# Kernel tuning notes

Hardware: AMD Instinct MI355X
Metric: run time of the kernel (lower is better)

## Reference

```python
import jax, jax.numpy as jnp
import numpy as np

N = 128
HID = 512
NUM_IRREPS = 7

_ISO = np.array([
    [1,0,1,0,0,0,0],
    [0,1,0,1,1,0,0],
    [1,0,1,0,0,0,0],
    [0,1,0,1,1,0,0],
    [0,1,0,1,1,0,0],
    [0,0,0,0,0,1,0],
    [0,0,0,0,0,0,1],
], dtype=np.float32)


def setup_inputs() -> dict:
    key = jax.random.key(0)
    k1, k2 = jax.random.split(key)
    x = jax.random.normal(k1, (2, N, N, HID), dtype=jnp.float32)
    # xavier_uniform with relu gain on [num_irreps, num_irreps]
    gain = float(np.sqrt(2.0))
    bound = gain * float(np.sqrt(6.0 / (NUM_IRREPS + NUM_IRREPS)))
    weight = jax.random.uniform(k2, (NUM_IRREPS, NUM_IRREPS), dtype=jnp.float32,
                                minval=-bound, maxval=bound)
    iso_matrix = jnp.asarray(_ISO)
    return {"x": x, "weight": weight, "iso_matrix": iso_matrix}


def _decompose(M):
    # M: [h, n, n] -> [7, h, n, n], isotypic components under S_n conjugation.
    n = M.shape[-1]
    eye = jnp.eye(n, dtype=M.dtype)
    off = 1.0 - eye
    d = jnp.diagonal(M, axis1=-2, axis2=-1)                 # [h, n]
    dbar = jnp.mean(d, axis=-1, keepdims=True)              # [h, 1]
    P1 = dbar[..., None] * eye                              # diag mean (trivial)
    P2 = (d - dbar)[..., None] * eye                        # diag deviation (standard)
    O = M * off                                             # off-diagonal part
    s = jnp.sum(O, axis=(-2, -1)) / (n * (n - 1))           # [h]
    P3 = s[..., None, None] * off                           # offdiag mean (trivial)
    Op = O - P3
    r = jnp.sum(Op, axis=-1)                                # row sums, [h, n]
    c = jnp.sum(Op, axis=-2)                                # col sums, [h, n]
    xr = ((n - 1) * r + c) / (n * (n - 2))
    yc = ((n - 1) * c + r) / (n * (n - 2))
    P4 = xr[..., :, None] * off                             # row standard copy
    P5 = yc[..., None, :] * off                             # col standard copy
    R = Op - P4 - P5                                        # zero diag / row / col sums
    Rt = jnp.swapaxes(R, -1, -2)
    P6 = 0.5 * (R + Rt)                                     # irrep (n-2,2)
    P7 = 0.5 * (R - Rt)                                     # irrep (n-2,1,1)
    return jnp.stack([P1, P2, P3, P4, P5, P6, P7])          # [7, h, n, n]


def reference(x, weight, iso_matrix):
    # x: [2, n, n, hidden] -> transpose(1,3): [2, hidden, n, n]
    xt = jnp.transpose(x, (0, 3, 2, 1))
    A, B = xt[0], xt[1]                                     # [h, n, n]
    params = weight * iso_matrix                            # [7, 7]
    a = _decompose(A)                                       # [7, h, n, n]
    b = _decompose(B)
    # params @ comps, then sum over output irrep axis (fused into one einsum)
    A_out = jnp.einsum('ij,jhmn->hmn', params, a)
    B_out = jnp.einsum('ij,jhmn->hmn', params, b)
    out = jnp.stack([A_out, B_out])                         # [2, h, n, n]
    return jnp.transpose(out, (0, 3, 2, 1))                 # [2, n, n, hidden]
```

## Files before the change

kernel.cpp:

```cpp
#include <hip/hip_runtime.h>
#include <math.h>

#define N 128
#define HID 512
#define NH (N * HID)
#define SNH ((size_t)N * NH)
#define NPAIRS (N * (N + 1) / 2)

#define OFF_PSC 0
#define OFF_PSR 4194304
#define OFF_DG  4718592
#define OFF_XR  4849664
#define OFF_YC  4980736
#define OFF_SV  5111808
#define OFF_DB  5112832

typedef float vf4 __attribute__((ext_vector_type(4)));
union F4 { vf4 v; float f[4]; };

__global__ __launch_bounds__(512)
void schur_p1(const float* __restrict__ x, float* __restrict__ PScol,
              float* __restrict__ PSrow, float* __restrict__ Dg) {
    const int u  = blockIdx.x;
    const int hq = u & 3;
    const int bq = (u >> 2) & 3;
    const int g  = (u >> 4) & 7;
    const int s  = u >> 7;
    const int tid = threadIdx.x;
    const int f   = tid & 31;
    const int bg  = tid >> 5;
    const int b0  = bq * 32 + bg * 2;
    const int hoff = hq * 128 + f * 4;

    const float* xs   = x + (size_t)s * SNH;
    const float* base = xs + (size_t)(g * 16) * NH + b0 * HID + hoff;

    __shared__ F4 rowred[8][16][32];

    F4 acc0, acc1;
    acc0.v = (vf4)(0.f); acc1.v = (vf4)(0.f);

    #pragma unroll
    for (int c = 0; c < 2; ++c) {
        #pragma unroll
        for (int al = 0; al < 8; ++al) {
            const float* p = base + (size_t)(c * 8 + al) * NH;
            F4 v0; v0.v = *reinterpret_cast<const vf4*>(p);
            F4 v1; v1.v = *reinterpret_cast<const vf4*>(p + HID);
            acc0.v += v0.v;
            acc1.v += v1.v;
            F4 rs; rs.v = v0.v + v1.v;
            rowred[al][bg][f] = rs;
        }
        __syncthreads();
        if (tid < 256) {
            const int ar = tid >> 5;
            const int f2 = tid & 31;
            F4 t; t.v = (vf4)(0.f);
            #pragma unroll
            for (int k = 0; k < 16; ++k) t.v += rowred[ar][k][f2].v;
            const int a = g * 16 + c * 8 + ar;
            *reinterpret_cast<vf4*>(PSrow +
                ((((size_t)s * 4 + bq) * N + a) * HID + hq * 128 + f2 * 4)) = t.v;
        }
        __syncthreads();
    }

    *reinterpret_cast<vf4*>(PScol +
        ((((size_t)s * 8 + g) * N + b0) * HID + hoff)) = acc0.v;
    *reinterpret_cast<vf4*>(PScol +
        ((((size_t)s * 8 + g) * N + b0 + 1) * HID + hoff)) = acc1.v;

    if (bq == (g >> 1)) {
        const int ar = tid >> 5;
        const int f2 = tid & 31;
        const int a  = g * 16 + ar;
        const vf4 dv = *reinterpret_cast<const vf4*>(
            xs + (size_t)a * NH + a * HID + hq * 128 + f2 * 4);
        *reinterpret_cast<vf4*>(Dg +
            (((size_t)s * N + a) * HID + hq * 128 + f2 * 4)) = dv;
    }
}

__global__ __launch_bounds__(512)
void schur_p2(const float* __restrict__ PScol, const float* __restrict__ PSrow,
              const float* __restrict__ Dg,
              float* __restrict__ Xr, float* __restrict__ Yc,
              float* __restrict__ Sv, float* __restrict__ Db) {
    const int bi = blockIdx.x;
    const int s  = bi >> 4;
    const int hc = bi & 15;
    const int t  = threadIdx.x;
    const int iq = t >> 5;
    const int hl = t & 31;
    const int h  = hc * 32 + hl;

    float sa8[8], sb8[8], d8[8];
    float T = 0.f, D = 0.f;
    #pragma unroll
    for (int k = 0; k < 8; ++k) {
        const int i = iq + k * 16;
        float sa = 0.f, sb = 0.f;
        #pragma unroll
        for (int gg = 0; gg < 8; ++gg)
            sa += PScol[(((size_t)s * 8 + gg) * N + i) * HID + h];
        #pragma unroll
        for (int qq = 0; qq < 4; ++qq)
            sb += PSrow[(((size_t)s * 4 + qq) * N + i) * HID + h];
        const float d = Dg[((size_t)s * N + i) * HID + h];
        sa8[k] = sa; sb8[k] = sb; d8[k] = d;
        T += sa; D += d;
    }

    __shared__ float redT[16][32];
    __shared__ float redD[16][32];
    __shared__ float shS[32];
    redT[iq][hl] = T;
    redD[iq][hl] = D;
    __syncthreads();
    if (iq == 0) {
        float Tt = 0.f, Dd = 0.f;
        #pragma unroll
        for (int q = 0; q < 16; ++q) { Tt += redT[q][hl]; Dd += redD[q][hl]; }
        const float sh   = (Tt - Dd) * (1.0f / 16256.0f);
        const float dbar = Dd * (1.0f / 128.0f);
        Sv[s * HID + h] = sh;
        Db[s * HID + h] = dbar;
        shS[hl] = sh;
    }
    __syncthreads();

    const float sh    = shS[hl];
    const float k127s = 127.0f * sh;
    const float inv   = 1.0f / 16128.0f;
    const size_t base = (size_t)s * N * HID;
    #pragma unroll
    for (int k = 0; k < 8; ++k) {
        const int i = iq + k * 16;
        const float d = d8[k];
        const float r = sa8[k] - d - k127s;
        const float c = sb8[k] - d - k127s;
        Xr[base + (size_t)i * HID + h] = (127.0f * r + c) * inv;
        Yc[base + (size_t)i * HID + h] = (127.0f * c + r) * inv;
    }
}

__global__ __launch_bounds__(256)
void schur_p3(const float* __restrict__ x, const float* __restrict__ w,
              const float* __restrict__ iso,
              const float* __restrict__ Xr, const float* __restrict__ Yc,
              const float* __restrict__ Sv, const float* __restrict__ Db,
              float* __restrict__ out) {
    const int t  = threadIdx.x;
    const int k  = t >> 7;
    const int ht = t & 127;
    const int hoff = ht * 4;

    float c[7];
    #pragma unroll
    for (int j = 0; j < 7; ++j) {
        float acc = 0.f;
        #pragma unroll
        for (int i = 0; i < 7; ++i) acc += w[i * 7 + j] * iso[i * 7 + j];
        c[j] = acc;
    }
    const float c1 = c[0], c2 = c[1], c3 = c[2], c4 = c[3], c5 = c[4];
    const float al = 0.5f * (c[5] + c[6]);
    const float be = 0.5f * (c[5] - c[6]);

    const int pg0 = blockIdx.x * 8;

    #define TRI_OFF(aa) ((aa) * N - (((aa) * ((aa) - 1)) >> 1))
    #pragma unroll
    for (int it = 0; it < 4; ++it) {
        const int pg = pg0 + it * 2 + k;
        const int s  = (pg >= NPAIRS) ? 1 : 0;
        const int p  = pg - s * NPAIRS;

        int a = (int)((257.0f - sqrtf((float)(66049 - 8 * p))) * 0.5f);
        if (a < 0) a = 0;
        if (a > N - 1) a = N - 1;
        while (a > 0 && TRI_OFF(a) > p) --a;
        while (TRI_OFF(a + 1) <= p) ++a;
        const int b = a + (p - TRI_OFF(a));

        const size_t sbase    = (size_t)s * SNH;
        const size_t statbase = (size_t)s * N * HID;

        if (a == b) {
            F4 v;  v.v  = *reinterpret_cast<const vf4*>(x + sbase + ((size_t)a * N + a) * HID + hoff);
            F4 db; db.v = *reinterpret_cast<const vf4*>(Db + (size_t)s * HID + hoff);
            F4 o;
            #pragma unroll
            for (int j = 0; j < 4; ++j)
                o.f[j] = c1 * db.f[j] + c2 * (v.f[j] - db.f[j]);
            __builtin_nontemporal_store(o.v,
                reinterpret_cast<vf4*>(out + sbase + ((size_t)a * N + a) * HID + hoff));
            continue;
        }

        F4 va;  va.v  = *reinterpret_cast<const vf4*>(x + sbase + ((size_t)a * N + b) * HID + hoff);
        F4 vb;  vb.v  = *reinterpret_cast<const vf4*>(x + sbase + ((size_t)b * N + a) * HID + hoff);
        F4 xra; xra.v = *reinterpret_cast<const vf4*>(Xr + statbase + (size_t)a * HID + hoff);
        F4 xrb; xrb.v = *reinterpret_cast<const vf4*>(Xr + statbase + (size_t)b * HID + hoff);
        F4 yca; yca.v = *reinterpret_cast<const vf4*>(Yc + statbase + (size_t)a * HID + hoff);
        F4 ycb; ycb.v = *reinterpret_cast<const vf4*>(Yc + statbase + (size_t)b * HID + hoff);
        F4 sh;  sh.v  = *reinterpret_cast<const vf4*>(Sv + (size_t)s * HID + hoff);

        F4 oab, oba;
        #pragma unroll
        for (int j = 0; j < 4; ++j) {
            const float U = va.f[j] - sh.f[j] - xrb.f[j] - yca.f[j];
            const float V = vb.f[j] - sh.f[j] - xra.f[j] - ycb.f[j];
            oab.f[j] = c3 * sh.f[j] + c4 * xrb.f[j] + c5 * yca.f[j] + al * U + be * V;
            oba.f[j] = c3 * sh.f[j] + c4 * xra.f[j] + c5 * ycb.f[j] + al * V + be * U;
        }
        __builtin_nontemporal_store(oab.v,
            reinterpret_cast<vf4*>(out + sbase + ((size_t)a * N + b) * HID + hoff));
        __builtin_nontemporal_store(oba.v,
            reinterpret_cast<vf4*>(out + sbase + ((size_t)b * N + a) * HID + hoff));
    }
}

extern "C" void kernel_launch(void* const* d_in, const int* in_sizes, int n_in,
                              void* d_out, int out_size, void* d_ws, size_t ws_size,
                              hipStream_t stream) {
    const float* x   = (const float*)d_in[0];
    const float* w   = (const float*)d_in[1];
    const float* iso = (const float*)d_in[2];
    float* out = (float*)d_out;
    float* ws  = (float*)d_ws;

    float* PScol = ws + OFF_PSC;
    float* PSrow = ws + OFF_PSR;
    float* Dg    = ws + OFF_DG;
    float* Xr    = ws + OFF_XR;
    float* Yc    = ws + OFF_YC;
    float* Sv    = ws + OFF_SV;
    float* Db    = ws + OFF_DB;

    schur_p1<<<256, 512, 0, stream>>>(x, PScol, PSrow, Dg);
    schur_p2<<<32, 512, 0, stream>>>(PScol, PSrow, Dg, Xr, Yc, Sv, Db);
    schur_p3<<<2064, 256, 0, stream>>>(x, w, iso, Xr, Yc, Sv, Db, out);
}
```

Measured before the change: 45.78 us.

## Retile reduction pass into 8x8 tiles over full hidden width

```diff
diff --git a/kernel.cpp b/kernel.cpp
--- a/kernel.cpp
+++ b/kernel.cpp
@@ -8,77 +8,71 @@
 #define NPAIRS (N * (N + 1) / 2)
 
 #define OFF_PSC 0
-#define OFF_PSR 4194304
-#define OFF_DG  4718592
-#define OFF_XR  4849664
-#define OFF_YC  4980736
-#define OFF_SV  5111808
-#define OFF_DB  5112832
+#define OFF_PSR 2097152
+#define OFF_DG  4194304
+#define OFF_XR  4325376
+#define OFF_YC  4456448
+#define OFF_SV  4587520
+#define OFF_DB  4588544
 
 typedef float vf4 __attribute__((ext_vector_type(4)));
 union F4 { vf4 v; float f[4]; };
 
-__global__ __launch_bounds__(512)
+__global__ __launch_bounds__(256, 8)
 void schur_p1(const float* __restrict__ x, float* __restrict__ PScol,
               float* __restrict__ PSrow, float* __restrict__ Dg) {
-    const int u  = blockIdx.x;
-    const int hq = u & 3;
-    const int bq = (u >> 2) & 3;
-    const int g  = (u >> 4) & 7;
-    const int s  = u >> 7;
+    const int u   = blockIdx.x;
+    const int bg  = u & 15;
+    const int ag  = (u >> 4) & 15;
+    const int s   = u >> 8;
     const int tid = threadIdx.x;
-    const int f   = tid & 31;
-    const int bg  = tid >> 5;
-    const int b0  = bq * 32 + bg * 2;
-    const int hoff = hq * 128 + f * 4;
+    const int f   = tid & 127;
+    const int bh  = tid >> 7;
+    const int hoff = f * 4;
+    const int b0   = bg * 8 + bh * 4;
 
     const float* xs   = x + (size_t)s * SNH;
-    const float* base = xs + (size_t)(g * 16) * NH + b0 * HID + hoff;
-
-    __shared__ F4 rowred[8][16][32];
-
-    F4 acc0, acc1;
-    acc0.v = (vf4)(0.f); acc1.v = (vf4)(0.f);
-
-    #pragma unroll
-    for (int c = 0; c < 2; ++c) {
-        #pragma unroll
-        for (int al = 0; al < 8; ++al) {
-            const float* p = base + (size_t)(c * 8 + al) * NH;
-            F4 v0; v0.v = *reinterpret_cast<const vf4*>(p);
-            F4 v1; v1.v = *reinterpret_cast<const vf4*>(p + HID);
-            acc0.v += v0.v;
-            acc1.v += v1.v;
-            F4 rs; rs.v = v0.v + v1.v;
-            rowred[al][bg][f] = rs;
+    const float* base = xs + (size_t)(ag * 8) * NH + b0 * HID + hoff;
+    const bool diag = (ag == bg);
+
+    __shared__ F4 rowall[8][2][128];
+
+    F4 c0, c1, c2, c3;
+    c0.v = (vf4)(0.f); c1.v = (vf4)(0.f); c2.v = (vf4)(0.f); c3.v = (vf4)(0.f);
+
+    #pragma unroll
+    for (int ai = 0; ai < 8; ++ai) {
+        const float* p = base + (size_t)ai * NH;
+        F4 v0; v0.v = *reinterpret_cast<const vf4*>(p);
+        F4 v1; v1.v = *reinterpret_cast<const vf4*>(p + HID);
+        F4 v2; v2.v = *reinterpret_cast<const vf4*>(p + 2 * HID);
+        F4 v3; v3.v = *reinterpret_cast<const vf4*>(p + 3 * HID);
+        c0.v += v0.v; c1.v += v1.v; c2.v += v2.v; c3.v += v3.v;
+        F4 rs; rs.v = (v0.v + v1.v) + (v2.v + v3.v);
+        rowall[ai][bh][f] = rs;
+        if (diag && (ai >> 2) == bh) {
+            const int a = ag * 8 + ai;
+            F4 dv;
+            if ((ai & 3) == 0)      dv = v0;
+            else if ((ai & 3) == 1) dv = v1;
+            else if ((ai & 3) == 2) dv = v2;
+            else                    dv = v3;
+            *reinterpret_cast<vf4*>(Dg + (((size_t)s * N + a) * HID + hoff)) = dv.v;
         }
-        __syncthreads();
-        if (tid < 256) {
-            const int ar = tid >> 5;
-            const int f2 = tid & 31;
-            F4 t; t.v = (vf4)(0.f);
-            #pragma unroll
-            for (int k = 0; k < 16; ++k) t.v += rowred[ar][k][f2].v;
-            const int a = g * 16 + c * 8 + ar;
-            *reinterpret_cast<vf4*>(PSrow +
-                ((((size_t)s * 4 + bq) * N + a) * HID + hq * 128 + f2 * 4)) = t.v;
-        }
-        __syncthreads();
-    }
-
-    *reinterpret_cast<vf4*>(PScol +
-        ((((size_t)s * 8 + g) * N + b0) * HID + hoff)) = acc0.v;
-    *reinterpret_cast<vf4*>(PScol +
-        ((((size_t)s * 8 + g) * N + b0 + 1) * HID + hoff)) = acc1.v;
-
-    if (bq == (g >> 1)) {
-        const int ar = tid >> 5;
-        const int f2 = tid & 31;
-        const int a  = g * 16 + ar;
-        const vf4 dv = *reinterpret_cast<const vf4*>(
-            xs + (size_t)a * NH + a * HID + hq * 128 + f2 * 4);
-        *reinterpret_cast<vf4*>(Dg +
-            (((size_t)s * N + a) * HID + hq * 128 + f2 * 4)) = dv;
+    }
+    __syncthreads();
+
+    *reinterpret_cast<vf4*>(PScol + ((((size_t)s * 16 + ag) * N + b0 + 0) * HID + hoff)) = c0.v;
+    *reinterpret_cast<vf4*>(PScol + ((((size_t)s * 16 + ag) * N + b0 + 1) * HID + hoff)) = c1.v;
+    *reinterpret_cast<vf4*>(PScol + ((((size_t)s * 16 + ag) * N + b0 + 2) * HID + hoff)) = c2.v;
+    *reinterpret_cast<vf4*>(PScol + ((((size_t)s * 16 + ag) * N + b0 + 3) * HID + hoff)) = c3.v;
+
+    #pragma unroll
+    for (int k = 0; k < 4; ++k) {
+        const int ai = bh + 2 * k;
+        F4 t; t.v = rowall[ai][0][f].v + rowall[ai][1][f].v;
+        *reinterpret_cast<vf4*>(PSrow +
+            ((((size_t)s * 16 + bg) * N + ag * 8 + ai) * HID + hoff)) = t.v;
     }
 }
 
@@ -102,11 +96,11 @@
         const int i = iq + k * 16;
         float sa = 0.f, sb = 0.f;
         #pragma unroll
-        for (int gg = 0; gg < 8; ++gg)
-            sa += PScol[(((size_t)s * 8 + gg) * N + i) * HID + h];
-        #pragma unroll
-        for (int qq = 0; qq < 4; ++qq)
-            sb += PSrow[(((size_t)s * 4 + qq) * N + i) * HID + h];
+        for (int gg = 0; gg < 16; ++gg)
+            sa += PScol[(((size_t)s * 16 + gg) * N + i) * HID + h];
+        #pragma unroll
+        for (int qq = 0; qq < 16; ++qq)
+            sb += PSrow[(((size_t)s * 16 + qq) * N + i) * HID + h];
         const float d = Dg[((size_t)s * N + i) * HID + h];
         sa8[k] = sa; sb8[k] = sb; d8[k] = d;
         T += sa; D += d;
@@ -239,7 +233,7 @@
     float* Sv    = ws + OFF_SV;
     float* Db    = ws + OFF_DB;
 
-    schur_p1<<<256, 512, 0, stream>>>(x, PScol, PSrow, Dg);
+    schur_p1<<<512, 256, 0, stream>>>(x, PScol, PSrow, Dg);
     schur_p2<<<32, 512, 0, stream>>>(PScol, PSrow, Dg, Xr, Yc, Sv, Db);
     schur_p3<<<2064, 256, 0, stream>>>(x, w, iso, Xr, Yc, Sv, Db, out);
 }
```

Measured after the change: 52.83 us. +15.4%, slower.
